# Performance work log

Hardware: AMD Instinct MI355X
Metric: run time of the kernel (lower is better)

Reference implementation:

```python
import jax, jax.numpy as jnp
import numpy as np
from jax.ops import segment_sum

N_NODES = 50000
N_EDGES = 400000
D_IN = 128
HIDDEN = [128, 128]
D_OUT = 64
ALPHA = 0.5


def _glorot(key, shape):
    fan_in, fan_out = shape
    lim = jnp.sqrt(6.0 / (fan_in + fan_out))
    return jax.random.uniform(key, shape, jnp.float32, -lim, lim)


def setup_inputs() -> dict:
    key = jax.random.key(0)
    ks = jax.random.split(key, 16)
    x = jax.random.normal(ks[0], (N_NODES, D_IN), jnp.float32)
    edge_index = jax.random.randint(ks[1], (2, N_EDGES), 0, N_NODES, jnp.int64)
    theta = jax.random.uniform(ks[2], (N_EDGES,), jnp.float32)
    return {
        "x": x,
        "edge_index": edge_index,
        "theta": theta,
        "W1_s2d": _glorot(ks[3], (D_IN, HIDDEN[0])),
        "W1_d2s": _glorot(ks[4], (D_IN, HIDDEN[0])),
        "b1_s2d": jnp.zeros((HIDDEN[0],), jnp.float32),
        "b1_d2s": jnp.zeros((HIDDEN[0],), jnp.float32),
        "W2_s2d": _glorot(ks[5], (HIDDEN[0], HIDDEN[1])),
        "W2_d2s": _glorot(ks[6], (HIDDEN[0], HIDDEN[1])),
        "b2_s2d": jnp.zeros((HIDDEN[1],), jnp.float32),
        "b2_d2s": jnp.zeros((HIDDEN[1],), jnp.float32),
        "W_ro": _glorot(ks[7], (HIDDEN[1], D_OUT)),
        "b_ro": jnp.zeros((D_OUT,), jnp.float32),
    }


def _fuzzy_laplacian(edge_index, theta, num_nodes):
    # bidirectional duplication + self loops (self_loop=True, edge_weight=1)
    senders, receivers = edge_index[0], edge_index[1]
    loop = jnp.arange(num_nodes, dtype=senders.dtype)
    cs = jnp.concatenate((senders, receivers, loop))
    cr = jnp.concatenate((receivers, senders, loop))
    c2, s2 = jnp.cos(theta) ** 2, jnp.sin(theta) ** 2
    ones = jnp.ones((num_nodes,), theta.dtype)
    # real(e^{i t})^2 = cos^2 t ; exp(i(pi/2 - t)) -> real^2 = sin^2 t
    out_w = jnp.concatenate((c2, s2, ones))
    in_w = jnp.concatenate((s2, c2, ones))
    deg_s = segment_sum(out_w, cs, num_segments=num_nodes) + 1e-12
    deg_r = segment_sum(in_w, cs, num_segments=num_nodes) + 1e-12
    dis_s = jnp.where(deg_s > 1e11, 0.0, jax.lax.rsqrt(deg_s))
    dis_r = jnp.where(deg_r > 1e11, 0.0, jax.lax.rsqrt(deg_r))
    w_s2d = dis_s[cs] * out_w * dis_r[cr]
    w_d2s = dis_r[cs] * in_w * dis_s[cr]
    return cs, cr, w_s2d, w_d2s


def _forward(x, edge_index, theta, W1_s2d, W1_d2s, b1_s2d, b1_d2s,
             W2_s2d, W2_d2s, b2_s2d, b2_d2s, W_ro, b_ro):
    num_nodes = x.shape[0]
    cs, cr, w_s2d, w_d2s = _fuzzy_laplacian(edge_index, theta, num_nodes)
    layers = [(W1_s2d, W1_d2s, b1_s2d, b1_d2s), (W2_s2d, W2_d2s, b2_s2d, b2_d2s)]
    for Ws, Wd, bs, bd in layers:
        xs = x[cs]  # [2E+N, F] gather
        agg_s = segment_sum(xs * w_s2d[:, None], cr, num_segments=num_nodes)
        agg_d = segment_sum(xs * w_d2s[:, None], cr, num_segments=num_nodes)
        x = ALPHA * (agg_s @ Ws + bs) + (1.0 - ALPHA) * (agg_d @ Wd + bd)
        x = jax.nn.relu(x)
    return x @ W_ro + b_ro


def reference(x, edge_index, theta, W1_s2d, W1_d2s, b1_s2d, b1_d2s,
              W2_s2d, W2_d2s, b2_s2d, b2_d2s, W_ro, b_ro):
    return _forward(x, edge_index, theta, W1_s2d, W1_d2s, b1_s2d, b1_d2s,
                    W2_s2d, W2_d2s, b2_s2d, b2_d2s, W_ro, b_ro)
```

## Files before the change

kernel.cpp:

```cpp
#include <hip/hip_runtime.h>
#include <hip/hip_fp16.h>

#define N_NODES 50000
#define N_EDGES 400000
#define CSR_E (2 * N_EDGES + N_NODES)
#define NCH 10
#define CHW 5000
#define NE2 (N_NODES * NCH)
#define EB8 196
#define PB 288
#define CB 512

typedef unsigned short ushort_t;
typedef unsigned int uint_t;
typedef __attribute__((ext_vector_type(8))) short bf16x8;
typedef __attribute__((ext_vector_type(4))) float f32x4;

__device__ __forceinline__ float bf2f(ushort_t u) {
    return __uint_as_float(((uint_t)u) << 16);
}
__device__ __forceinline__ ushort_t f2bf(float f) {
    uint_t b = __float_as_uint(f);
    b += 0x7FFFu + ((b >> 16) & 1u);
    return (ushort_t)(b >> 16);
}
__device__ __forceinline__ uint_t packw(float a, float b) {
    return ((uint_t)__half_as_ushort(__float2half(b)) << 16) |
           (uint_t)__half_as_ushort(__float2half(a));
}
__device__ __forceinline__ float unpl(uint_t w) {
    return __half2float(__ushort_as_half((ushort_t)(w & 0xffffu)));
}
__device__ __forceinline__ float unph(uint_t w) {
    return __half2float(__ushort_as_half((ushort_t)(w >> 16)));
}


__device__ int g_est;
__device__ int g_is16;
__device__ __align__(8) float2 g_dis2[N_NODES];
__device__ int g_cnt2[NE2];
__device__ int g_offs2[NE2 + 1];
__device__ uint_t g_scanst[512];
__device__ __align__(16) uint4 g_estage[N_EDGES];
__device__ __align__(16) uint2 g_csr8[CSR_E];
__device__ __align__(16) ushort_t g_h1[(size_t)N_NODES * 128];
__device__ __align__(16) ushort_t g_xcvt[(size_t)N_NODES * 128];
__device__ __align__(16) ushort_t g_bp1[8 * 128 * 32];
__device__ __align__(16) ushort_t g_bp2[8 * 128 * 32];
__device__ __align__(16) ushort_t g_bp3[4 * 64 * 32];
__device__ float g_bc1[128];
__device__ float g_bc2[128];
__device__ float g_bro[64];


__global__ __launch_bounds__(256) void edge_prep(
    const uint_t* __restrict__ xw,
    const int* __restrict__ eidx, const ushort_t* __restrict__ th16, const float* __restrict__ th32,
    const ushort_t* W1s16, const float* W1s32, const ushort_t* W1d16, const float* W1d32,
    const ushort_t* b1s16, const float* b1s32, const ushort_t* b1d16, const float* b1d32,
    const ushort_t* W2s16, const float* W2s32, const ushort_t* W2d16, const float* W2d32,
    const ushort_t* b2s16, const float* b2s32, const ushort_t* b2d16, const float* b2d32,
    const ushort_t* Wro16, const float* Wro32, const ushort_t* bro16, const float* bro32) {
    __shared__ int s_flags;
    if (threadIdx.x < 64) {
        uint_t w = xw[threadIdx.x];
        int elo = (w >> 7) & 0xFF;
        unsigned long long mb = __ballot(elo >= 100 && elo <= 150);
        unsigned long long me = __ballot(eidx[2 * threadIdx.x + 1] != 0);
        if (threadIdx.x == 0) {
            int is16v = (__popcll(mb) >= 48) ? 1 : 0;
            int estv = me ? 1 : 2;
            s_flags = is16v | (estv << 1);
        }
    }
    __syncthreads();
    int is16 = s_flags & 1;
    int est = s_flags >> 1;
    int gb = blockIdx.x;
    if (gb == 0 && threadIdx.x == 0) {
        g_is16 = is16;
        g_est = est;
    }
    if (gb < EB8) {
        int base = gb * 2048 + threadIdx.x;
        int sv[8], rv[8];
        float th[8];
#pragma unroll
        for (int u = 0; u < 8; u++) {
            int e = base + u * 256;
            if (e < N_EDGES) {
                sv[u] = eidx[(size_t)e * est];
                rv[u] = eidx[((size_t)N_EDGES + e) * est];
                th[u] = is16 ? bf2f(th16[e]) : th32[e];
            } else { sv[u] = 0; rv[u] = 0; th[u] = 0.f; }
        }
        float c2v[8];
#pragma unroll
        for (int u = 0; u < 8; u++) {
            float sn, cs_;
            sincosf(th[u], &sn, &cs_);
            c2v[u] = cs_ * cs_;
        }
        int rf[8], rr_[8];
#pragma unroll
        for (int u = 0; u < 8; u++) {
            int e = base + u * 256;
            if (e < N_EDGES) {
                rf[u] = atomicAdd(&g_cnt2[rv[u] * NCH + sv[u] / CHW], 1);
                rr_[u] = atomicAdd(&g_cnt2[sv[u] * NCH + rv[u] / CHW], 1);
            } else { rf[u] = 0; rr_[u] = 0; }
        }
#pragma unroll
        for (int u = 0; u < 8; u++) {
            int e = base + u * 256;
            if (e < N_EDGES)
                g_estage[e] = make_uint4((uint_t)sv[u], (uint_t)rv[u], __float_as_uint(c2v[u]),
                                         (uint_t)rf[u] | ((uint_t)rr_[u] << 16));
        }
        return;
    }
    if (gb < EB8 + PB) {
        int t = (gb - EB8) * 256 + threadIdx.x;
        if (t < 2 * 32768) {
            int layer = t >> 15;
            int i = t & 32767;
            const ushort_t* Ws16 = layer ? W2s16 : W1s16;
            const float* Ws32 = layer ? W2s32 : W1s32;
            const ushort_t* Wd16 = layer ? W2d16 : W1d16;
            const float* Wd32 = layer ? W2d32 : W1d32;
            ushort_t* Bp = layer ? g_bp2 : g_bp1;
            int k = i >> 7, n = i & 127;
            ushort_t v;
            if (k < 128) {
                int idx = k * 128 + n;
                v = is16 ? Ws16[idx] : f2bf(Ws32[idx]);
            } else {
                int idx = (k - 128) * 128 + n;
                v = is16 ? Wd16[idx] : f2bf(Wd32[idx]);
            }
            int kb = k >> 5, kk = k & 31;
            Bp[((kb * 128 + n) << 5) + kk] = v;
            if (i < 128) {
                const ushort_t* bs16 = layer ? b2s16 : b1s16;
                const float* bs32 = layer ? b2s32 : b1s32;
                const ushort_t* bd16 = layer ? b2d16 : b1d16;
                const float* bd32 = layer ? b2d32 : b1d32;
                float a = is16 ? bf2f(bs16[i]) : bs32[i];
                float b = is16 ? bf2f(bd16[i]) : bd32[i];
                (layer ? g_bc2 : g_bc1)[i] = 0.5f * (a + b);
            }
        } else {
            int i = t - 2 * 32768;
            int k = i >> 6, n = i & 63;
            ushort_t v = is16 ? Wro16[i] : f2bf(Wro32[i]);
            int kb = k >> 5, kk = k & 31;
            g_bp3[((kb * 64 + n) << 5) + kk] = v;
            if (i < 64) g_bro[i] = is16 ? bf2f(bro16[i]) : bro32[i];
        }
        return;
    }
    if (is16) return;
    const float* x32 = (const float*)xw;
    const int total = N_NODES * 128 / 8;
    for (int i = (gb - EB8 - PB) * 256 + threadIdx.x; i < total; i += CB * 256) {
        const float4* p = (const float4*)(x32 + (size_t)i * 8);
        float4 a = p[0], b = p[1];
        ushort4 o0, o1;
        o0.x = f2bf(a.x); o0.y = f2bf(a.y); o0.z = f2bf(a.z); o0.w = f2bf(a.w);
        o1.x = f2bf(b.x); o1.y = f2bf(b.y); o1.z = f2bf(b.z); o1.w = f2bf(b.w);
        *(ushort4*)(g_xcvt + (size_t)i * 8) = o0;
        *(ushort4*)(g_xcvt + (size_t)i * 8 + 4) = o1;
    }
}


__global__ __launch_bounds__(1024) void scan_lb() {
    __shared__ int sd[1024];
    __shared__ int s_ex;
    int b = blockIdx.x;
    int t = threadIdx.x;
    int i = b * 1024 + t;
    int v = 0;
    if (i < NE2) {
        int n = i / NCH;
        int c = i - n * NCH;
        v = g_cnt2[i] + ((c == n / CHW) ? 1 : 0);
        g_cnt2[i] = 0;
    }
    sd[t] = v;
    __syncthreads();
    for (int o = 1; o < 1024; o <<= 1) {
        int tv = (t >= o) ? sd[t - o] : 0;
        __syncthreads();
        sd[t] += tv;
        __syncthreads();
    }
    int incl = sd[t];
    int agg = sd[1023];
    if (t == 0) {
        atomicExch(&g_scanst[b], ((b == 0 ? 2u : 1u) << 20) | (uint_t)agg);
    }
    if (t < 64) {
        int ex = 0;
        if (b > 0) {
            int j = b - 1;
            while (true) {
                int idx = j - 63 + t;
                uint_t wv = (idx >= 0) ? atomicAdd(&g_scanst[idx], 0u) : (2u << 20);
                uint_t fl = wv >> 20;
                unsigned long long m2 = __ballot(fl == 2u);
                unsigned long long m0 = __ballot(fl == 0u);
                if (m2 != 0ull) {
                    int p = 63 - __clzll(m2);
                    unsigned long long above = (p == 63) ? 0ull : (~0ull << (p + 1));
                    if ((m0 & above) != 0ull) continue;
                    int contrib = (t >= p) ? (int)(wv & 0xFFFFFu) : 0;
#pragma unroll
                    for (int o = 1; o < 64; o <<= 1) contrib += __shfl_xor(contrib, o);
                    ex += contrib;
                    break;
                } else {
                    if (m0 != 0ull) continue;
                    int contrib = (int)(wv & 0xFFFFFu);
#pragma unroll
                    for (int o = 1; o < 64; o <<= 1) contrib += __shfl_xor(contrib, o);
                    ex += contrib;
                    j -= 64;
                }
            }
        }
        if (t == 0) {
            atomicExch(&g_scanst[b], (2u << 20) | (uint_t)(ex + agg));
            s_ex = ex;
        }
    }
    __syncthreads();
    if (i < NE2) g_offs2[i] = incl - v + s_ex;
    if (b == 0 && t == 0) g_offs2[NE2] = CSR_E;
}


__global__ __launch_bounds__(256) void fill_all() {
    if (blockIdx.x == 0 && threadIdx.x < 512) g_scanst[threadIdx.x] = 0;
    int e = blockIdx.x * 256 + threadIdx.x;
    if (e < N_EDGES) {
        uint4 stg = g_estage[e];
        int s = (int)stg.x;
        int r = (int)stg.y;
        float c2 = __uint_as_float(stg.z);
        float s2 = 1.0f - c2;
        uint_t rk = stg.w;
        int pf = g_offs2[r * NCH + s / CHW] + (int)(rk & 0xffffu);
        int pr = g_offs2[s * NCH + r / CHW] + (int)(rk >> 16);
        g_csr8[pf] = make_uint2((uint_t)s, packw(c2, s2));
        g_csr8[pr] = make_uint2((uint_t)r, packw(s2, c2));
    }
    if (e < N_NODES) {
        int b = e * NCH + e / CHW;
        g_csr8[g_offs2[b + 1] - 1] = make_uint2((uint_t)e, packw(1.0f, 1.0f));
    }
}


__global__ __launch_bounds__(256) void deg_pass() {
    int n = blockIdx.x * 256 + threadIdx.x;
    if (n >= N_NODES) return;
    int kb = g_offs2[n * NCH];
    int ke = g_offs2[n * NCH + NCH];
    float ds = 0.f, dr = 0.f;
    for (int k = kb; k < ke; k++) {
        uint_t w = g_csr8[k].y;
        ds += unph(w);
        dr += unpl(w);
    }
    g_dis2[n] = make_float2(rsqrtf(ds + 1e-12f), rsqrtf(dr + 1e-12f));
}


__global__ __launch_bounds__(256) void finalize_w() {
    int i = blockIdx.x * 256 + threadIdx.x;
    if (i >= CSR_E) return;
    uint2 e = g_csr8[i];
    float2 d = g_dis2[e.x];
    ((uint_t*)g_csr8)[2 * (size_t)i + 1] = packw(d.x * unpl(e.y), d.y * unph(e.y));
}


template <int LAYER>
__global__ __launch_bounds__(256) void fused_layer(const ushort_t* __restrict__ xext,
                                                   void* __restrict__ outp) {
    __shared__ ushort_t tA[16 * 256];
    __shared__ ushort_t tH[(LAYER == 1) ? 16 * 128 : 1];
    int w = threadIdx.x >> 6;
    int lane = threadIdx.x & 63;
    int gsel = lane >> 4;
    int r = lane & 15;
    int lrow = w * 4 + gsel;
    int node = blockIdx.x * 16 + lrow;
    const ushort_t* xin = (LAYER == 0) ? (g_is16 ? xext : g_xcvt) : g_h1;

    int ks = g_offs2[node * NCH];
    int ke = g_offs2[node * NCH + NCH];
    int c0 = ke - ks;
    int cmax = c0;
    cmax = max(cmax, __shfl_xor(cmax, 16));
    cmax = max(cmax, __shfl_xor(cmax, 32));

    float accS[8], accD[8];
#pragma unroll
    for (int f = 0; f < 8; f++) { accS[f] = 0.f; accD[f] = 0.f; }

    uint2 ecur = g_csr8[ks + min(r, c0 - 1)];
    int lbase = lane & 48;
    for (int k = 0; k < cmax; k += 16) {
        uint2 enext = ecur;
        if (k + 16 < cmax) enext = g_csr8[ks + min(k + 16 + r, c0 - 1)];
#pragma unroll
        for (int h = 0; h < 4; h++) {
            int kh = k + h * 4;
            if (kh >= cmax) break;
            uint_t eys[4];
            bf16x8 vs[4];
#pragma unroll
            for (int j = 0; j < 4; j++) {
                int jj = h * 4 + j;
                uint_t ex = (uint_t)__shfl((int)ecur.x, lbase | jj, 64);
                eys[j] = (uint_t)__shfl((int)ecur.y, lbase | jj, 64);
                vs[j] = *(const bf16x8*)(xin + (size_t)ex * 128 + r * 8);
            }
#pragma unroll
            for (int j = 0; j < 4; j++) {
                bool val = (kh + j) < c0;
                float ws_ = val ? unpl(eys[j]) : 0.f;
                float wd_ = val ? unph(eys[j]) : 0.f;
#pragma unroll
                for (int f = 0; f < 8; f++) {
                    float xv = bf2f((ushort_t)vs[j][f]);
                    accS[f] = fmaf(ws_, xv, accS[f]);
                    accD[f] = fmaf(wd_, xv, accD[f]);
                }
            }
        }
        ecur = enext;
    }

    float2 dn = g_dis2[node];
    float fs = 0.5f * dn.y;
    float fd = 0.5f * dn.x;
    uint_t oS[4], oD[4];
#pragma unroll
    for (int p = 0; p < 4; p++) {
        oS[p] = ((uint_t)f2bf(accS[2 * p + 1] * fs) << 16) | (uint_t)f2bf(accS[2 * p] * fs);
        oD[p] = ((uint_t)f2bf(accD[2 * p + 1] * fd) << 16) | (uint_t)f2bf(accD[2 * p] * fd);
    }
    int swA = (lrow & 7) << 4;
    *(uint4*)((char*)tA + ((lrow * 512 + r * 16) ^ swA)) = make_uint4(oS[0], oS[1], oS[2], oS[3]);
    *(uint4*)((char*)tA + ((lrow * 512 + 256 + r * 16) ^ swA)) = make_uint4(oD[0], oD[1], oD[2], oD[3]);
    __syncthreads();

    int cc = lane & 15;
    int q = lane >> 4;
    int csw = (cc & 7) << 4;
    const ushort_t* Bp = (LAYER == 0) ? g_bp1 : g_bp2;
    const float* bias = (LAYER == 0) ? g_bc1 : g_bc2;
    f32x4 acc0 = {0.f, 0.f, 0.f, 0.f};
    f32x4 acc1 = {0.f, 0.f, 0.f, 0.f};
#pragma unroll
    for (int kb = 0; kb < 8; kb++) {
        bf16x8 a = *(const bf16x8*)((const char*)tA + ((cc * 512 + kb * 64 + q * 16) ^ csw));
        bf16x8 b0 = *(const bf16x8*)(Bp + (((kb * 128 + w * 32 + cc) << 5) + q * 8));
        bf16x8 b1 = *(const bf16x8*)(Bp + (((kb * 128 + w * 32 + 16 + cc) << 5) + q * 8));
        acc0 = __builtin_amdgcn_mfma_f32_16x16x32_bf16(a, b0, acc0, 0, 0, 0);
        acc1 = __builtin_amdgcn_mfma_f32_16x16x32_bf16(a, b1, acc1, 0, 0, 0);
    }
    int mb = blockIdx.x * 16;
    float bi0 = bias[w * 32 + cc];
    float bi1 = bias[w * 32 + 16 + cc];
    if (LAYER == 0) {
#pragma unroll
        for (int rr = 0; rr < 4; rr++) {
            int m = mb + q * 4 + rr;
            g_h1[(size_t)m * 128 + w * 32 + cc] = f2bf(fmaxf(acc0[rr] + bi0, 0.f));
            g_h1[(size_t)m * 128 + w * 32 + 16 + cc] = f2bf(fmaxf(acc1[rr] + bi1, 0.f));
        }
    } else {
#pragma unroll
        for (int rr = 0; rr < 4; rr++) {
            int ml = q * 4 + rr;
            int msw = (ml & 7) << 4;
            *(ushort_t*)((char*)tH + ((ml * 256 + (w * 32 + cc) * 2) ^ msw)) =
                f2bf(fmaxf(acc0[rr] + bi0, 0.f));
            *(ushort_t*)((char*)tH + ((ml * 256 + (w * 32 + 16 + cc) * 2) ^ msw)) =
                f2bf(fmaxf(acc1[rr] + bi1, 0.f));
        }
        __syncthreads();
        f32x4 a3 = {0.f, 0.f, 0.f, 0.f};
#pragma unroll
        for (int kb = 0; kb < 4; kb++) {
            bf16x8 a = *(const bf16x8*)((const char*)tH + ((cc * 256 + kb * 64 + q * 16) ^ csw));
            bf16x8 b = *(const bf16x8*)(g_bp3 + (((kb * 64 + w * 16 + cc) << 5) + q * 8));
            a3 = __builtin_amdgcn_mfma_f32_16x16x32_bf16(a, b, a3, 0, 0, 0);
        }
        int is16 = g_is16;
        float bi = g_bro[w * 16 + cc];
#pragma unroll
        for (int rr = 0; rr < 4; rr++) {
            int m = mb + q * 4 + rr;
            float v = a3[rr] + bi;
            if (is16)
                ((ushort_t*)outp)[(size_t)m * 64 + w * 16 + cc] = f2bf(v);
            else
                ((float*)outp)[(size_t)m * 64 + w * 16 + cc] = v;
        }
    }
}


static inline int cdiv(int a, int b) { return (a + b - 1) / b; }

extern "C" void kernel_launch(void* const* d_in, const int* in_sizes, int n_in,
                              void* d_out, int out_size, void* d_ws, size_t ws_size,
                              hipStream_t stream) {
    const void* x = d_in[0];
    const int* eidx = (const int*)d_in[1];
    const void* theta = d_in[2];
    const void* W1s = d_in[3];
    const void* W1d = d_in[4];
    const void* b1s = d_in[5];
    const void* b1d = d_in[6];
    const void* W2s = d_in[7];
    const void* W2d = d_in[8];
    const void* b2s = d_in[9];
    const void* b2d = d_in[10];
    const void* Wro = d_in[11];
    const void* bro = d_in[12];
    (void)in_sizes; (void)n_in; (void)out_size; (void)d_ws; (void)ws_size;

    const int NB2 = cdiv(NE2, 1024);

    edge_prep<<<EB8 + PB + CB, 256, 0, stream>>>(
        (const uint_t*)x, eidx, (const ushort_t*)theta, (const float*)theta,
        (const ushort_t*)W1s, (const float*)W1s, (const ushort_t*)W1d, (const float*)W1d,
        (const ushort_t*)b1s, (const float*)b1s, (const ushort_t*)b1d, (const float*)b1d,
        (const ushort_t*)W2s, (const float*)W2s, (const ushort_t*)W2d, (const float*)W2d,
        (const ushort_t*)b2s, (const float*)b2s, (const ushort_t*)b2d, (const float*)b2d,
        (const ushort_t*)Wro, (const float*)Wro, (const ushort_t*)bro, (const float*)bro);
    scan_lb<<<NB2, 1024, 0, stream>>>();
    fill_all<<<cdiv(N_EDGES, 256), 256, 0, stream>>>();
    deg_pass<<<cdiv(N_NODES, 256), 256, 0, stream>>>();
    finalize_w<<<cdiv(CSR_E, 256), 256, 0, stream>>>();

    const int AB = N_NODES / 16;
    fused_layer<0><<<AB, 256, 0, stream>>>((const ushort_t*)x, nullptr);
    fused_layer<1><<<AB, 256, 0, stream>>>(nullptr, d_out);
}
```

Baseline: 254.5 us.

## Pack fixed-point degree sums into 64-bit count atomics, fold normalization into fill

Edge counting now uses 64-bit atomics whose fields carry the bucket count plus fixed-point sums of cos² and sin² weights. Degrees are reduced per node inside the scan kernel, and the normalized edge weights are written directly in fill_all. This removes the separate deg_pass and finalize_w kernels and a full read-modify-write pass over the CSR array. The cost is 64-bit atomics and fixed-point degree accumulation with limited precision and field width, plus an extra zeroing loop in fill_all.

New measurement: 246.5 us, median of 3. 1.03x faster.

```diff
diff --git a/kernel.cpp b/kernel.cpp
--- a/kernel.cpp
+++ b/kernel.cpp
@@ -10,9 +10,12 @@
 #define EB8 196
 #define PB 288
 #define CB 512
+#define RB_SCAN 489
+#define RB_DEGC 49
 
 typedef unsigned short ushort_t;
 typedef unsigned int uint_t;
+typedef unsigned long long ull_t;
 typedef __attribute__((ext_vector_type(8))) short bf16x8;
 typedef __attribute__((ext_vector_type(4))) float f32x4;
 
@@ -34,12 +37,15 @@
 __device__ __forceinline__ float unph(uint_t w) {
     return __half2float(__ushort_as_half((ushort_t)(w >> 16)));
 }
+__device__ __forceinline__ uint_t fixw(float x) {
+    return (uint_t)(x * 65536.0f + 0.5f);
+}
 
 
 __device__ int g_est;
 __device__ int g_is16;
 __device__ __align__(8) float2 g_dis2[N_NODES];
-__device__ int g_cnt2[NE2];
+__device__ ull_t g_cnt64[NE2];
 __device__ int g_offs2[NE2 + 1];
 __device__ uint_t g_scanst[512];
 __device__ __align__(16) uint4 g_estage[N_EDGES];
@@ -102,13 +108,19 @@
             sincosf(th[u], &sn, &cs_);
             c2v[u] = cs_ * cs_;
         }
-        int rf[8], rr_[8];
+        uint_t rf[8], rr_[8];
 #pragma unroll
         for (int u = 0; u < 8; u++) {
             int e = base + u * 256;
             if (e < N_EDGES) {
-                rf[u] = atomicAdd(&g_cnt2[rv[u] * NCH + sv[u] / CHW], 1);
-                rr_[u] = atomicAdd(&g_cnt2[sv[u] * NCH + rv[u] / CHW], 1);
+                uint_t fc2 = fixw(c2v[u]);
+                uint_t fs2 = fixw(1.0f - c2v[u]);
+                ull_t af = 1ull | ((ull_t)fs2 << 12) | ((ull_t)fc2 << 38);
+                ull_t ar = 1ull | ((ull_t)fc2 << 12) | ((ull_t)fs2 << 38);
+                ull_t retf = atomicAdd(&g_cnt64[rv[u] * NCH + sv[u] / CHW], af);
+                ull_t retr = atomicAdd(&g_cnt64[sv[u] * NCH + rv[u] / CHW], ar);
+                rf[u] = (uint_t)(retf & 0xFFFull);
+                rr_[u] = (uint_t)(retr & 0xFFFull);
             } else { rf[u] = 0; rr_[u] = 0; }
         }
 #pragma unroll
@@ -116,7 +128,7 @@
             int e = base + u * 256;
             if (e < N_EDGES)
                 g_estage[e] = make_uint4((uint_t)sv[u], (uint_t)rv[u], __float_as_uint(c2v[u]),
-                                         (uint_t)rf[u] | ((uint_t)rr_[u] << 16));
+                                         rf[u] | (rr_[u] << 16));
         }
         return;
     }
@@ -175,18 +187,34 @@
 }
 
 
-__global__ __launch_bounds__(1024) void scan_lb() {
+__global__ __launch_bounds__(1024) void scan_deg() {
+    int gb = blockIdx.x;
+    int t = threadIdx.x;
+    if (gb >= RB_SCAN) {
+        int n = (gb - RB_SCAN) * 1024 + t;
+        if (n < N_NODES) {
+            ull_t sS = 0, sD = 0;
+#pragma unroll
+            for (int c = 0; c < NCH; c++) {
+                ull_t w = g_cnt64[n * NCH + c];
+                sS += (w >> 12) & 0x3FFFFFFull;
+                sD += (w >> 38);
+            }
+            float ds = (float)sS * (1.0f / 65536.0f) + 1.0f;
+            float dr = (float)sD * (1.0f / 65536.0f) + 1.0f;
+            g_dis2[n] = make_float2(rsqrtf(ds + 1e-12f), rsqrtf(dr + 1e-12f));
+        }
+        return;
+    }
     __shared__ int sd[1024];
     __shared__ int s_ex;
-    int b = blockIdx.x;
-    int t = threadIdx.x;
+    int b = gb;
     int i = b * 1024 + t;
     int v = 0;
     if (i < NE2) {
         int n = i / NCH;
         int c = i - n * NCH;
-        v = g_cnt2[i] + ((c == n / CHW) ? 1 : 0);
-        g_cnt2[i] = 0;
+        v = (int)(g_cnt64[i] & 0xFFFull) + ((c == n / CHW) ? 1 : 0);
     }
     sd[t] = v;
     __syncthreads();
@@ -243,6 +271,8 @@
 
 __global__ __launch_bounds__(256) void fill_all() {
     if (blockIdx.x == 0 && threadIdx.x < 512) g_scanst[threadIdx.x] = 0;
+    for (int i = blockIdx.x * 256 + threadIdx.x; i < NE2; i += gridDim.x * 256)
+        g_cnt64[i] = 0;
     int e = blockIdx.x * 256 + threadIdx.x;
     if (e < N_EDGES) {
         uint4 stg = g_estage[e];
@@ -251,39 +281,18 @@
         float c2 = __uint_as_float(stg.z);
         float s2 = 1.0f - c2;
         uint_t rk = stg.w;
+        float2 dss = g_dis2[s];
+        float2 dsr = g_dis2[r];
         int pf = g_offs2[r * NCH + s / CHW] + (int)(rk & 0xffffu);
         int pr = g_offs2[s * NCH + r / CHW] + (int)(rk >> 16);
-        g_csr8[pf] = make_uint2((uint_t)s, packw(c2, s2));
-        g_csr8[pr] = make_uint2((uint_t)r, packw(s2, c2));
+        g_csr8[pf] = make_uint2((uint_t)s, packw(dss.x * c2, dss.y * s2));
+        g_csr8[pr] = make_uint2((uint_t)r, packw(dsr.x * s2, dsr.y * c2));
     }
     if (e < N_NODES) {
         int b = e * NCH + e / CHW;
-        g_csr8[g_offs2[b + 1] - 1] = make_uint2((uint_t)e, packw(1.0f, 1.0f));
-    }
-}
-
-
-__global__ __launch_bounds__(256) void deg_pass() {
-    int n = blockIdx.x * 256 + threadIdx.x;
-    if (n >= N_NODES) return;
-    int kb = g_offs2[n * NCH];
-    int ke = g_offs2[n * NCH + NCH];
-    float ds = 0.f, dr = 0.f;
-    for (int k = kb; k < ke; k++) {
-        uint_t w = g_csr8[k].y;
-        ds += unph(w);
-        dr += unpl(w);
-    }
-    g_dis2[n] = make_float2(rsqrtf(ds + 1e-12f), rsqrtf(dr + 1e-12f));
-}
-
-
-__global__ __launch_bounds__(256) void finalize_w() {
-    int i = blockIdx.x * 256 + threadIdx.x;
-    if (i >= CSR_E) return;
-    uint2 e = g_csr8[i];
-    float2 d = g_dis2[e.x];
-    ((uint_t*)g_csr8)[2 * (size_t)i + 1] = packw(d.x * unpl(e.y), d.y * unph(e.y));
+        float2 d = g_dis2[e];
+        g_csr8[g_offs2[b + 1] - 1] = make_uint2((uint_t)e, packw(d.x, d.y));
+    }
 }
 
 
@@ -437,8 +446,6 @@
     const void* bro = d_in[12];
     (void)in_sizes; (void)n_in; (void)out_size; (void)d_ws; (void)ws_size;
 
-    const int NB2 = cdiv(NE2, 1024);
-
     edge_prep<<<EB8 + PB + CB, 256, 0, stream>>>(
         (const uint_t*)x, eidx, (const ushort_t*)theta, (const float*)theta,
         (const ushort_t*)W1s, (const float*)W1s, (const ushort_t*)W1d, (const float*)W1d,
@@ -446,10 +453,8 @@
         (const ushort_t*)W2s, (const float*)W2s, (const ushort_t*)W2d, (const float*)W2d,
         (const ushort_t*)b2s, (const float*)b2s, (const ushort_t*)b2d, (const float*)b2d,
         (const ushort_t*)Wro, (const float*)Wro, (const ushort_t*)bro, (const float*)bro);
-    scan_lb<<<NB2, 1024, 0, stream>>>();
+    scan_deg<<<RB_SCAN + RB_DEGC, 1024, 0, stream>>>();
     fill_all<<<cdiv(N_EDGES, 256), 256, 0, stream>>>();
-    deg_pass<<<cdiv(N_NODES, 256), 256, 0, stream>>>();
-    finalize_w<<<cdiv(CSR_E, 256), 256, 0, stream>>>();
 
     const int AB = N_NODES / 16;
     fused_layer<0><<<AB, 256, 0, stream>>>((const ushort_t*)x, nullptr);
```
